# Kernel tuning notes

Hardware: AMD Instinct MI355X
Metric: run time of the kernel (lower is better)

## Reference

```python
import jax, jax.numpy as jnp
import numpy as np

MATRY_DIMS = (64, 128, 256, 512, 768)   # nested matryoshka prefix dims
TEMPERATURE = 0.05                      # SimCSE default
REL_IMPORTANCE = np.ones(len(MATRY_DIMS), dtype=np.float32)
EPS = 1e-8                              # torch cosine_similarity eps


def _contrastive_loss_one_dim(emb1, emb2, d):
    # prefix-slice to matryoshka dim d, cosine-sim matrix, softmax CE vs arange labels
    a = emb1[:, :d]
    b = emb2[:, :d]
    a = a / jnp.maximum(jnp.linalg.norm(a, axis=-1, keepdims=True), EPS)
    b = b / jnp.maximum(jnp.linalg.norm(b, axis=-1, keepdims=True), EPS)
    logits = jnp.einsum('id,jd->ij', a, b) / TEMPERATURE  # [N, N]
    logp = jax.nn.log_softmax(logits, axis=-1)
    # CrossEntropyLoss with labels = arange(N): mean of -logp[i, i]
    return -jnp.mean(jnp.diagonal(logp))


def setup_inputs() -> dict:
    key = jax.random.key(0)
    k1, k2 = jax.random.split(key)
    N, D = 8192, 768
    return {
        'emb1': jax.random.normal(k1, (N, D), dtype=jnp.float32),
        'emb2': jax.random.normal(k2, (N, D), dtype=jnp.float32),
    }


def reference(emb1, emb2):
    losses = jnp.stack([_contrastive_loss_one_dim(emb1, emb2, d) for d in MATRY_DIMS])
    weighted = jnp.asarray(REL_IMPORTANCE) * losses
    return jnp.sum(weighted)
```

## Files before the change

kernel.cpp:

```cpp
#include <hip/hip_runtime.h>
#include <math.h>

typedef __attribute__((ext_vector_type(4))) float f32x4;
typedef __attribute__((ext_vector_type(8))) int   i32x8;

#define N_ROWS 8192
#define DFULL 768
#define KSC (1.4426950408889634f / 0.05f)
#define NEGSH (-28.853900817779268f)
#define LN2 0.6931471805599453f
#define PLB32 ((size_t)N_ROWS * 32)
#define EXPA 8388608.0f
#define FEXPC ((NEGSH + 126.9427f) * 8388608.0f)
#define DIAGC (LN2 / 8388608.0f)

__global__ __launch_bounds__(192) void mcl_prep(
    const float* __restrict__ e1, const float* __restrict__ e2,
    char* __restrict__ h1, char* __restrict__ h2,
    float* __restrict__ inv1, float* __restrict__ inv2)
{
  const int b = blockIdx.x;
  const int mat = b >> 13, row = b & (N_ROWS - 1);
  const float* src = (mat ? e2 : e1) + (size_t)row * DFULL;
  char* dst = mat ? h2 : h1;
  float* invo = mat ? inv2 : inv1;
  const int t = threadIdx.x;
  const int k = t * 4;

  const f32x4 v = *(const f32x4*)(src + k);
  const float s = v[0]*v[0] + v[1]*v[1] + v[2]*v[2] + v[3]*v[3];
  float p0 = (k < 64)  ? s : 0.f;
  float p1 = (k < 128) ? s : 0.f;
  float p2 = (k < 256) ? s : 0.f;
  float p3 = (k < 512) ? s : 0.f;
  float p4 = s;

  const int lo = __builtin_amdgcn_cvt_pk_fp8_f32(v[0], v[1], 0, false);
  const int pk = __builtin_amdgcn_cvt_pk_fp8_f32(v[2], v[3], lo, true);
  *(int*)(dst + (size_t)(k >> 5) * PLB32 + (size_t)row * 32 + (k & 31)) = pk;

#pragma unroll
  for (int off = 32; off > 0; off >>= 1) {
    p0 += __shfl_down(p0, off, 64);
    p1 += __shfl_down(p1, off, 64);
    p2 += __shfl_down(p2, off, 64);
    p3 += __shfl_down(p3, off, 64);
    p4 += __shfl_down(p4, off, 64);
  }
  __shared__ float red[3][5];
  const int lane = t & 63, w = t >> 6;
  if (lane == 0) { red[w][0]=p0; red[w][1]=p1; red[w][2]=p2; red[w][3]=p3; red[w][4]=p4; }
  __syncthreads();
  if (t == 0) {
#pragma unroll
    for (int q = 0; q < 5; ++q) {
      const float sum = red[0][q] + red[1][q] + red[2][q];
      invo[q * N_ROWS + row] = 1.f / fmaxf(sqrtf(sum), 1e-8f);
    }
  }
}

__global__ __launch_bounds__(256, 2) void mcl_main(
    const char* __restrict__ h1, const char* __restrict__ h2,
    const float* __restrict__ inv1, const float* __restrict__ inv2,
    float* __restrict__ diag, float* __restrict__ partial)
{
  __shared__ float rowsumW[2][5][128];

  const int tid = threadIdx.x;
  const int lane = tid & 63, wid = tid >> 6;
  const int wr = wid >> 1, wc = wid & 1;
  const int l15 = lane & 15, lh = lane >> 4;
  const int rgd = l15 & 3;

  const int id = blockIdx.x;
  const int nid = (id & 7) * 512 + (id >> 3);
  const int st = nid >> 6, tt = nid & 63;
  const int bi = ((st >> 3) << 3) + (tt >> 3);
  const int bj = ((st & 7) << 3) + (tt & 7);
  const int rowA0 = bi * 128, rowB0 = bj * 128;
  const bool dgb = (bi == bj) && (wr == wc) && (lh == (l15 >> 2));

  const char* pa = h1 + (size_t)lh * PLB32 + (size_t)(rowA0 + wr * 64 + l15) * 32;
  const char* pb = h2 + (size_t)lh * PLB32 + (size_t)(rowB0 + wc * 64 + l15) * 32;

  f32x4 acc[4][4];
#pragma unroll
  for (int n = 0; n < 4; ++n)
#pragma unroll
    for (int m = 0; m < 4; ++m) acc[n][m] = (f32x4)0.f;

#define LOADF(CK) do {                                                         \
    _Pragma("unroll")                                                          \
    for (int m = 0; m < 4; ++m) {                                              \
      af[m] = *(const i32x8*)(pa + (CK) * 4 * PLB32 + m * 512);                \
      bf[m] = *(const i32x8*)(pb + (CK) * 4 * PLB32 + m * 512);                \
    } } while (0)

#define MFMACL() do {                                                          \
    __builtin_amdgcn_s_setprio(1);                                             \
    _Pragma("unroll")                                                          \
    for (int n = 0; n < 4; ++n)                                                \
      _Pragma("unroll")                                                        \
      for (int m = 0; m < 4; ++m)                                              \
        acc[n][m] = __builtin_amdgcn_mfma_scale_f32_16x16x128_f8f6f4(          \
            bf[n], af[m], acc[n][m], 0, 0, 0, 0x7F, 0, 0x7F);                  \
    __builtin_amdgcn_s_setprio(0);                                             \
  } while (0)

#define SUMEXP(RP, T, S1M) do {                                                \
    const f32x4 ub = (T) * (S1M) + FEXPC;                                      \
    RP += __int_as_float((int)ub[0]) + __int_as_float((int)ub[1]) +            \
          __int_as_float((int)ub[2]) + __int_as_float((int)ub[3]); } while (0)

#define REDUCE_STORE(RP, DCP) do {                                             \
    _Pragma("unroll")                                                          \
    for (int m = 0; m < 4; ++m) {                                              \
      float v_ = (RP)[m];                                                      \
      v_ += __shfl_xor(v_, 16, 64);                                            \
      v_ += __shfl_xor(v_, 32, 64);                                            \
      if (lh == 0) rowsumW[wc][(DCP)][wr * 64 + m * 16 + l15] = v_;            \
    } } while (0)

#define EPIPRE(DCP, S1, S2) do {                                               \
    _Pragma("unroll")                                                          \
    for (int m = 0; m < 4; ++m)                                                \
      S1[m] = inv1[(DCP) * N_ROWS + rowA0 + wr * 64 + m * 16 + l15]            \
              * (KSC * EXPA);                                                  \
    _Pragma("unroll")                                                          \
    for (int n = 0; n < 4; ++n)                                                \
      S2[n] = *(const f32x4*)(inv2 + (DCP) * N_ROWS + rowB0 + wc * 64 +        \
                              n * 16 + (lh << 2));                             \
  } while (0)

#define EPIMAIN(DCP, S1, S2) do {                                              \
    float rp[4] = {0.f, 0.f, 0.f, 0.f};                                        \
    _Pragma("unroll")                                                          \
    for (int n = 0; n < 4; ++n)                                                \
      _Pragma("unroll")                                                        \
      for (int m = 0; m < 4; ++m) {                                            \
        const f32x4 t = acc[n][m] * S2[n];                                     \
        SUMEXP(rp[m], t, S1[m]);                                               \
      }                                                                        \
    REDUCE_STORE(rp, (DCP));                                                   \
    if (dgb) {                                                                 \
      _Pragma("unroll")                                                        \
      for (int m = 0; m < 4; ++m)                                              \
        diag[(DCP) * N_ROWS + rowA0 + wr * 64 + m * 16 + l15] =                \
            acc[m][m][rgd] * S1[m] * S2[m][rgd] * DIAGC;                       \
    } } while (0)

  i32x8 af[4], bf[4];

  {
    float s1a[4]; f32x4 s2a[4];
    EPIPRE(0, s1a, s2a);
    LOADF(0);
    const int msk = (lh < 2) ? 0x7F : 0x00;
    float rp0[4] = {0.f, 0.f, 0.f, 0.f};
#pragma unroll
    for (int n = 0; n < 4; ++n) {
#pragma unroll
      for (int m = 0; m < 4; ++m) {
        const f32x4 t = __builtin_amdgcn_mfma_scale_f32_16x16x128_f8f6f4(
            bf[n], af[m], (f32x4)0.f, 0, 0, 0, msk, 0, msk);
        acc[n][m] = __builtin_amdgcn_mfma_scale_f32_16x16x128_f8f6f4(
            bf[n], af[m], acc[n][m], 0, 0, 0, 0x7F, 0, 0x7F);
        const f32x4 ts = t * s2a[n];
        SUMEXP(rp0[m], ts, s1a[m]);
        if (n == m && dgb)
          diag[0 * N_ROWS + rowA0 + wr * 64 + m * 16 + l15] =
              t[rgd] * s1a[m] * s2a[m][rgd] * DIAGC;
      }
    }
    REDUCE_STORE(rp0, 0);
  }

  {
    float s1b[4]; f32x4 s2b[4];
    EPIPRE(1, s1b, s2b);
    LOADF(1);
    EPIMAIN(1, s1b, s2b);
    MFMACL();
  }
  {
    float s1c[4]; f32x4 s2c[4];
    EPIPRE(2, s1c, s2c);
    LOADF(2);
    EPIMAIN(2, s1c, s2c);
    MFMACL();
  }
  {
    LOADF(3);
    MFMACL();
  }
  {
    float s1d[4]; f32x4 s2d4[4];
    EPIPRE(3, s1d, s2d4);
    LOADF(4);
    EPIMAIN(3, s1d, s2d4);
    MFMACL();
  }
  {
    float s1e[4]; f32x4 s2e[4];
    EPIPRE(4, s1e, s2e);
    LOADF(5);
    MFMACL();
    EPIMAIN(4, s1e, s2e);
  }

#undef EPIMAIN
#undef EPIPRE
#undef REDUCE_STORE
#undef SUMEXP
#undef MFMACL
#undef LOADF

  __syncthreads();
  for (int x = tid; x < 5 * 128; x += 256) {
    const int d = x >> 7, r = x & 127;
    atomicAdd(&partial[d * N_ROWS + rowA0 + r], rowsumW[0][d][r] + rowsumW[1][d][r]);
  }
}

__global__ __launch_bounds__(256) void mcl_reduce(
    const float* __restrict__ partial, const float* __restrict__ diag,
    float* __restrict__ out)
{
  const int item = blockIdx.x * 256 + threadIdx.x;
  const int d = item >> 13;
  const int i = item & (N_ROWS - 1);
  const float s = partial[d * N_ROWS + i];
  float term = (20.0f + logf(s) - diag[d * N_ROWS + i]) * (1.0f / 8192.0f);
#pragma unroll
  for (int off = 32; off > 0; off >>= 1) term += __shfl_down(term, off, 64);
  __shared__ float red[4];
  const int lane = threadIdx.x & 63, w = threadIdx.x >> 6;
  if (lane == 0) red[w] = term;
  __syncthreads();
  if (threadIdx.x == 0) atomicAdd(out, red[0] + red[1] + red[2] + red[3]);
}

extern "C" void kernel_launch(void* const* d_in, const int* in_sizes, int n_in,
                              void* d_out, int out_size, void* d_ws, size_t ws_size,
                              hipStream_t stream) {
  const float* e1 = (const float*)d_in[0];
  const float* e2 = (const float*)d_in[1];
  char* ws = (char*)d_ws;

  const size_t HBYTES = (size_t)N_ROWS * DFULL;
  const size_t IBYTES = (size_t)5 * N_ROWS * sizeof(float);
  char*  h1      = ws;
  char*  h2      = ws + HBYTES;
  float* inv1    = (float*)(ws + 2 * HBYTES);
  float* inv2    = (float*)(ws + 2 * HBYTES + IBYTES);
  float* diag    = (float*)(ws + 2 * HBYTES + 2 * IBYTES);
  float* partial = (float*)(ws + 2 * HBYTES + 3 * IBYTES);
  const size_t NEED = 2 * HBYTES + 4 * IBYTES;
  if (ws_size < NEED) return;

  hipMemsetAsync(d_out, 0, sizeof(float) * out_size, stream);
  hipMemsetAsync(partial, 0, IBYTES, stream);
  mcl_prep<<<2 * N_ROWS, 192, 0, stream>>>(e1, e2, h1, h2, inv1, inv2);
  mcl_main<<<4096, 256, 0, stream>>>(h1, h2, inv1, inv2, diag, partial);
  mcl_reduce<<<160, 256, 0, stream>>>(partial, diag, (float*)d_out);
}
```

Baseline: 121.6 us.

## Stage FP8 tiles through double-buffered LDS with async global-to-LDS loads

New measurement: 147.8 us. +21.5%, slower.

```diff
diff --git a/kernel.cpp b/kernel.cpp
--- a/kernel.cpp
+++ b/kernel.cpp
@@ -2,17 +2,24 @@
 #include <math.h>
 
 typedef __attribute__((ext_vector_type(4))) float f32x4;
+typedef __attribute__((ext_vector_type(4))) int   i32x4;
 typedef __attribute__((ext_vector_type(8))) int   i32x8;
+
+#define AS1 __attribute__((address_space(1)))
+#define AS3 __attribute__((address_space(3)))
 
 #define N_ROWS 8192
 #define DFULL 768
 #define KSC (1.4426950408889634f / 0.05f)
 #define NEGSH (-28.853900817779268f)
 #define LN2 0.6931471805599453f
-#define PLB32 ((size_t)N_ROWS * 32)
 #define EXPA 8388608.0f
 #define FEXPC ((NEGSH + 126.9427f) * 8388608.0f)
 #define DIAGC (LN2 / 8388608.0f)
+
+__device__ __forceinline__ void gload_lds16(const void* g, void* l) {
+  __builtin_amdgcn_global_load_lds((const AS1 void*)g, (AS3 void*)l, 16, 0, 0);
+}
 
 __global__ __launch_bounds__(192) void mcl_prep(
     const float* __restrict__ e1, const float* __restrict__ e2,
@@ -22,7 +29,7 @@
   const int b = blockIdx.x;
   const int mat = b >> 13, row = b & (N_ROWS - 1);
   const float* src = (mat ? e2 : e1) + (size_t)row * DFULL;
-  char* dst = mat ? h2 : h1;
+  char* dst = (mat ? h2 : h1) + (size_t)row * DFULL;
   float* invo = mat ? inv2 : inv1;
   const int t = threadIdx.x;
   const int k = t * 4;
@@ -37,7 +44,7 @@
 
   const int lo = __builtin_amdgcn_cvt_pk_fp8_f32(v[0], v[1], 0, false);
   const int pk = __builtin_amdgcn_cvt_pk_fp8_f32(v[2], v[3], lo, true);
-  *(int*)(dst + (size_t)(k >> 5) * PLB32 + (size_t)row * 32 + (k & 31)) = pk;
+  *(int*)(dst + k) = pk;
 
 #pragma unroll
   for (int off = 32; off > 0; off >>= 1) {
@@ -65,6 +72,7 @@
     const float* __restrict__ inv1, const float* __restrict__ inv2,
     float* __restrict__ diag, float* __restrict__ partial)
 {
+  __shared__ __align__(16) char smem[2][2][16384];
   __shared__ float rowsumW[2][5][128];
 
   const int tid = threadIdx.x;
@@ -72,6 +80,8 @@
   const int wr = wid >> 1, wc = wid & 1;
   const int l15 = lane & 15, lh = lane >> 4;
   const int rgd = l15 & 3;
+  const int r8 = lane >> 3;
+  const int sor = (lane & 7) ^ r8;
 
   const int id = blockIdx.x;
   const int nid = (id & 7) * 512 + (id >> 3);
@@ -81,20 +91,35 @@
   const int rowA0 = bi * 128, rowB0 = bj * 128;
   const bool dgb = (bi == bj) && (wr == wc) && (lh == (l15 >> 2));
 
-  const char* pa = h1 + (size_t)lh * PLB32 + (size_t)(rowA0 + wr * 64 + l15) * 32;
-  const char* pb = h2 + (size_t)lh * PLB32 + (size_t)(rowB0 + wc * 64 + l15) * 32;
-
   f32x4 acc[4][4];
 #pragma unroll
   for (int n = 0; n < 4; ++n)
 #pragma unroll
     for (int m = 0; m < 4; ++m) acc[n][m] = (f32x4)0.f;
 
-#define LOADF(CK) do {                                                         \
+#define STAGE(BUF, CK) do {                                                    \
+    _Pragma("unroll")                                                          \
+    for (int i = 0; i < 4; ++i) {                                              \
+      const int lrow = i * 32 + wid * 8 + r8;                                  \
+      gload_lds16(h1 + (size_t)(rowA0 + lrow) * DFULL + (CK) * 128 + sor * 16, \
+                  &smem[BUF][0][i * 4096 + wid * 1024]);                       \
+      gload_lds16(h2 + (size_t)(rowB0 + lrow) * DFULL + (CK) * 128 + sor * 16, \
+                  &smem[BUF][1][i * 4096 + wid * 1024]);                       \
+    } } while (0)
+
+#define FRAG(DST, BASE, ROWX) do {                                             \
+    const int s1_ = (((lh << 1) ^ ((ROWX) & 7)) << 4);                         \
+    const i32x4 lo_ = *(const i32x4*)((BASE) + (ROWX) * 128 + s1_);            \
+    const i32x4 hi_ = *(const i32x4*)((BASE) + (ROWX) * 128 + (s1_ ^ 16));     \
+    DST = __builtin_shufflevector(lo_, hi_, 0, 1, 2, 3, 4, 5, 6, 7); } while (0)
+
+#define LOADF(CUR) do {                                                        \
+    const char* bA_ = (const char*)smem[CUR][0];                               \
+    const char* bB_ = (const char*)smem[CUR][1];                               \
     _Pragma("unroll")                                                          \
     for (int m = 0; m < 4; ++m) {                                              \
-      af[m] = *(const i32x8*)(pa + (CK) * 4 * PLB32 + m * 512);                \
-      bf[m] = *(const i32x8*)(pb + (CK) * 4 * PLB32 + m * 512);                \
+      FRAG(af[m], bA_, wr * 64 + m * 16 + l15);                                \
+      FRAG(bf[m], bB_, wc * 64 + m * 16 + l15);                                \
     } } while (0)
 
 #define MFMACL() do {                                                          \
@@ -152,9 +177,13 @@
 
   i32x8 af[4], bf[4];
 
+  STAGE(0, 0);
+  __syncthreads();
+
   {
     float s1a[4]; f32x4 s2a[4];
     EPIPRE(0, s1a, s2a);
+    STAGE(1, 1);
     LOADF(0);
     const int msk = (lh < 2) ? 0x7F : 0x00;
     float rp0[4] = {0.f, 0.f, 0.f, 0.f};
@@ -174,37 +203,45 @@
       }
     }
     REDUCE_STORE(rp0, 0);
-  }
-
+    __syncthreads();
+  }
   {
     float s1b[4]; f32x4 s2b[4];
     EPIPRE(1, s1b, s2b);
+    STAGE(0, 2);
     LOADF(1);
     EPIMAIN(1, s1b, s2b);
     MFMACL();
+    __syncthreads();
   }
   {
     float s1c[4]; f32x4 s2c[4];
     EPIPRE(2, s1c, s2c);
-    LOADF(2);
+    STAGE(1, 3);
+    LOADF(0);
     EPIMAIN(2, s1c, s2c);
     MFMACL();
-  }
-  {
-    LOADF(3);
-    MFMACL();
+    __syncthreads();
+  }
+  {
+    STAGE(0, 4);
+    LOADF(1);
+    MFMACL();
+    __syncthreads();
   }
   {
     float s1d[4]; f32x4 s2d4[4];
     EPIPRE(3, s1d, s2d4);
-    LOADF(4);
+    STAGE(1, 5);
+    LOADF(0);
     EPIMAIN(3, s1d, s2d4);
     MFMACL();
+    __syncthreads();
   }
   {
     float s1e[4]; f32x4 s2e[4];
     EPIPRE(4, s1e, s2e);
-    LOADF(5);
+    LOADF(1);
     MFMACL();
     EPIMAIN(4, s1e, s2e);
   }
@@ -215,6 +252,8 @@
 #undef SUMEXP
 #undef MFMACL
 #undef LOADF
+#undef FRAG
+#undef STAGE
 
   __syncthreads();
   for (int x = tid; x < 5 * 128; x += 256) {
```

## Use one wave per row in prep and defer rowsum shuffles past MFMA issue

Applied to the files above, without the earlier changes.

After: 268.1 us. 2.21x slower.

```diff
diff --git a/kernel.cpp b/kernel.cpp
--- a/kernel.cpp
+++ b/kernel.cpp
@@ -14,31 +14,33 @@
 #define FEXPC ((NEGSH + 126.9427f) * 8388608.0f)
 #define DIAGC (LN2 / 8388608.0f)
 
-__global__ __launch_bounds__(192) void mcl_prep(
+__global__ __launch_bounds__(256) void mcl_prep(
     const float* __restrict__ e1, const float* __restrict__ e2,
     char* __restrict__ h1, char* __restrict__ h2,
     float* __restrict__ inv1, float* __restrict__ inv2)
 {
-  const int b = blockIdx.x;
+  const int w = threadIdx.x >> 6, lane = threadIdx.x & 63;
+  const int b = blockIdx.x * 4 + w;
   const int mat = b >> 13, row = b & (N_ROWS - 1);
   const float* src = (mat ? e2 : e1) + (size_t)row * DFULL;
   char* dst = mat ? h2 : h1;
   float* invo = mat ? inv2 : inv1;
-  const int t = threadIdx.x;
-  const int k = t * 4;
-
-  const f32x4 v = *(const f32x4*)(src + k);
-  const float s = v[0]*v[0] + v[1]*v[1] + v[2]*v[2] + v[3]*v[3];
-  float p0 = (k < 64)  ? s : 0.f;
-  float p1 = (k < 128) ? s : 0.f;
-  float p2 = (k < 256) ? s : 0.f;
-  float p3 = (k < 512) ? s : 0.f;
-  float p4 = s;
-
-  const int lo = __builtin_amdgcn_cvt_pk_fp8_f32(v[0], v[1], 0, false);
-  const int pk = __builtin_amdgcn_cvt_pk_fp8_f32(v[2], v[3], lo, true);
-  *(int*)(dst + (size_t)(k >> 5) * PLB32 + (size_t)row * 32 + (k & 31)) = pk;
-
+
+  float p0 = 0.f, p1 = 0.f, p2 = 0.f, p3 = 0.f, p4 = 0.f;
+#pragma unroll
+  for (int pass = 0; pass < 3; ++pass) {
+    const int k = pass * 256 + lane * 4;
+    const f32x4 v = *(const f32x4*)(src + k);
+    const float s = v[0]*v[0] + v[1]*v[1] + v[2]*v[2] + v[3]*v[3];
+    p0 += (k < 64)  ? s : 0.f;
+    p1 += (k < 128) ? s : 0.f;
+    p2 += (k < 256) ? s : 0.f;
+    p3 += (k < 512) ? s : 0.f;
+    p4 += s;
+    const int lo = __builtin_amdgcn_cvt_pk_fp8_f32(v[0], v[1], 0, false);
+    const int pk = __builtin_amdgcn_cvt_pk_fp8_f32(v[2], v[3], lo, true);
+    *(int*)(dst + (size_t)(k >> 5) * PLB32 + (size_t)row * 32 + (k & 31)) = pk;
+  }
 #pragma unroll
   for (int off = 32; off > 0; off >>= 1) {
     p0 += __shfl_down(p0, off, 64);
@@ -47,16 +49,12 @@
     p3 += __shfl_down(p3, off, 64);
     p4 += __shfl_down(p4, off, 64);
   }
-  __shared__ float red[3][5];
-  const int lane = t & 63, w = t >> 6;
-  if (lane == 0) { red[w][0]=p0; red[w][1]=p1; red[w][2]=p2; red[w][3]=p3; red[w][4]=p4; }
-  __syncthreads();
-  if (t == 0) {
-#pragma unroll
-    for (int q = 0; q < 5; ++q) {
-      const float sum = red[0][q] + red[1][q] + red[2][q];
-      invo[q * N_ROWS + row] = 1.f / fmaxf(sqrtf(sum), 1e-8f);
-    }
+  if (lane == 0) {
+    invo[0 * N_ROWS + row] = 1.f / fmaxf(sqrtf(p0), 1e-8f);
+    invo[1 * N_ROWS + row] = 1.f / fmaxf(sqrtf(p1), 1e-8f);
+    invo[2 * N_ROWS + row] = 1.f / fmaxf(sqrtf(p2), 1e-8f);
+    invo[3 * N_ROWS + row] = 1.f / fmaxf(sqrtf(p3), 1e-8f);
+    invo[4 * N_ROWS + row] = 1.f / fmaxf(sqrtf(p4), 1e-8f);
   }
 }
 
@@ -113,7 +111,7 @@
     RP += __int_as_float((int)ub[0]) + __int_as_float((int)ub[1]) +            \
           __int_as_float((int)ub[2]) + __int_as_float((int)ub[3]); } while (0)
 
-#define REDUCE_STORE(RP, DCP) do {                                             \
+#define RS(RP, DCP) do {                                                       \
     _Pragma("unroll")                                                          \
     for (int m = 0; m < 4; ++m) {                                              \
       float v_ = (RP)[m];                                                      \
@@ -133,16 +131,16 @@
                               n * 16 + (lh << 2));                             \
   } while (0)
 
-#define EPIMAIN(DCP, S1, S2) do {                                              \
-    float rp[4] = {0.f, 0.f, 0.f, 0.f};                                        \
+#define EPIEXP(DCP, S1, S2, RP) do {                                           \
+    _Pragma("unroll")                                                          \
+    for (int m = 0; m < 4; ++m) (RP)[m] = 0.f;                                 \
     _Pragma("unroll")                                                          \
     for (int n = 0; n < 4; ++n)                                                \
       _Pragma("unroll")                                                        \
       for (int m = 0; m < 4; ++m) {                                            \
         const f32x4 t = acc[n][m] * S2[n];                                     \
-        SUMEXP(rp[m], t, S1[m]);                                               \
+        SUMEXP((RP)[m], t, S1[m]);                                             \
       }                                                                        \
-    REDUCE_STORE(rp, (DCP));                                                   \
     if (dgb) {                                                                 \
       _Pragma("unroll")                                                        \
       for (int m = 0; m < 4; ++m)                                              \
@@ -151,6 +149,7 @@
     } } while (0)
 
   i32x8 af[4], bf[4];
+  float rpd[4];
 
   {
     float s1a[4]; f32x4 s2a[4];
@@ -173,45 +172,51 @@
               t[rgd] * s1a[m] * s2a[m][rgd] * DIAGC;
       }
     }
-    REDUCE_STORE(rp0, 0);
+    RS(rp0, 0);
   }
 
   {
     float s1b[4]; f32x4 s2b[4];
     EPIPRE(1, s1b, s2b);
     LOADF(1);
-    EPIMAIN(1, s1b, s2b);
+    float rp1[4];
+    EPIEXP(1, s1b, s2b, rp1);
+    RS(rp1, 1);
     MFMACL();
   }
   {
     float s1c[4]; f32x4 s2c[4];
     EPIPRE(2, s1c, s2c);
     LOADF(2);
-    EPIMAIN(2, s1c, s2c);
+    EPIEXP(2, s1c, s2c, rpd);
     MFMACL();
   }
   {
     LOADF(3);
+    RS(rpd, 2);
     MFMACL();
   }
   {
     float s1d[4]; f32x4 s2d4[4];
     EPIPRE(3, s1d, s2d4);
     LOADF(4);
-    EPIMAIN(3, s1d, s2d4);
+    EPIEXP(3, s1d, s2d4, rpd);
     MFMACL();
   }
   {
     float s1e[4]; f32x4 s2e[4];
     EPIPRE(4, s1e, s2e);
     LOADF(5);
-    MFMACL();
-    EPIMAIN(4, s1e, s2e);
-  }
-
-#undef EPIMAIN
+    RS(rpd, 3);
+    MFMACL();
+    float rp4[4];
+    EPIEXP(4, s1e, s2e, rp4);
+    RS(rp4, 4);
+  }
+
+#undef EPIEXP
 #undef EPIPRE
-#undef REDUCE_STORE
+#undef RS
 #undef SUMEXP
 #undef MFMACL
 #undef LOADF
@@ -261,7 +266,7 @@
 
   hipMemsetAsync(d_out, 0, sizeof(float) * out_size, stream);
   hipMemsetAsync(partial, 0, IBYTES, stream);
-  mcl_prep<<<2 * N_ROWS, 192, 0, stream>>>(e1, e2, h1, h2, inv1, inv2);
+  mcl_prep<<<4096, 256, 0, stream>>>(e1, e2, h1, h2, inv1, inv2);
   mcl_main<<<4096, 256, 0, stream>>>(h1, h2, inv1, inv2, diag, partial);
   mcl_reduce<<<160, 256, 0, stream>>>(partial, diag, (float*)d_out);
 }
```
